# Optimization experiments

Hardware: AMD Instinct MI355X
Metric: run time of the kernel (lower is better)

Reference implementation:

```python
import jax, jax.numpy as jnp
from jax import lax
import numpy as np

B, T, D, H, DH, FF, K = 16, 1024, 512, 8, 64, 2048, 3
EPS = 1e-5


def _layer_norm(x, g, b):
    mu = jnp.mean(x, axis=-1, keepdims=True)
    var = jnp.mean((x - mu) ** 2, axis=-1, keepdims=True)
    return (x - mu) / jnp.sqrt(var + EPS) * g + b


def setup_inputs() -> dict:
    key = jax.random.key(0)
    ks = jax.random.split(key, 14)
    f32 = jnp.float32
    dec_inp = jax.random.normal(ks[0], (B, T, D), f32)
    lengths = jax.random.randint(ks[1], (B,), T // 2, T + 1)
    mask = (jnp.arange(T)[None, :] < lengths[:, None])[:, :, None]  # [B,T,1] bool
    qkv_w = jax.random.normal(ks[2], (3 * H * DH, D), f32) * (D ** -0.5)
    qkv_b = jnp.zeros((3 * H * DH,), f32)
    o_w = jax.random.normal(ks[3], (D, H * DH), f32) * ((H * DH) ** -0.5)
    ln1_g = jnp.ones((D,), f32)
    ln1_b = jnp.zeros((D,), f32)
    conv1_w = jax.random.normal(ks[4], (FF, D, K), f32) * ((D * K) ** -0.5)
    conv1_b = jnp.zeros((FF,), f32)
    conv2_w = jax.random.normal(ks[5], (D, FF, K), f32) * ((FF * K) ** -0.5)
    conv2_b = jnp.zeros((D,), f32)
    ln2_g = jnp.ones((D,), f32)
    ln2_b = jnp.zeros((D,), f32)
    return dict(dec_inp=dec_inp, mask=mask, qkv_w=qkv_w, qkv_b=qkv_b, o_w=o_w,
                ln1_g=ln1_g, ln1_b=ln1_b, conv1_w=conv1_w, conv1_b=conv1_b,
                conv2_w=conv2_w, conv2_b=conv2_b, ln2_g=ln2_g, ln2_b=ln2_b)


def reference(dec_inp, mask, qkv_w, qkv_b, o_w, ln1_g, ln1_b,
              conv1_w, conv1_b, conv2_w, conv2_b, ln2_g, ln2_b):
    # ----- MultiHeadAttn (post-norm, dropout = identity in eval) -----
    attn_mask = ~mask[:, :, 0]                      # [B,T], True = pad
    qkv = dec_inp @ qkv_w.T + qkv_b                 # [B,T,3*H*DH]
    q, k, v = jnp.split(qkv, 3, axis=2)

    def to_heads(x):  # [B,T,H*DH] -> [B*H,T,DH] (batch-major, as in torch)
        return x.reshape(B, T, H, DH).transpose(0, 2, 1, 3).reshape(B * H, T, DH)

    q, k, v = to_heads(q), to_heads(k), to_heads(v)
    scores = jnp.einsum('bqd,bkd->bqk', q, k) * (DH ** -0.5)  # [B*H,T,T]
    # faithful to torch: mask tiled head-major (index i % B)
    am = jnp.tile(attn_mask[:, None, :], (H, T, 1))           # [B*H,T,T]
    scores = jnp.where(am, -jnp.inf, scores)
    prob = jax.nn.softmax(scores, axis=2)
    vec = jnp.einsum('bqk,bkd->bqd', prob, v)                 # [B*H,T,DH]
    # faithful to torch: view as [H,B,...] then permute
    vec = vec.reshape(H, B, T, DH).transpose(1, 2, 0, 3).reshape(B, T, H * DH)
    attn_out = vec @ o_w.T                                    # [B,T,D]
    out = _layer_norm(dec_inp + attn_out, ln1_g, ln1_b)
    out = out * mask

    # ----- PositionwiseConvFF (post-norm) -----
    x = out.transpose(0, 2, 1)                                # [B,D,T]
    h = lax.conv_general_dilated(x, conv1_w, (1,), [(K // 2, K // 2)],
                                 dimension_numbers=('NCH', 'OIH', 'NCH'))
    h = jax.nn.relu(h + conv1_b[None, :, None])
    h = lax.conv_general_dilated(h, conv2_w, (1,), [(K // 2, K // 2)],
                                 dimension_numbers=('NCH', 'OIH', 'NCH'))
    core = (h + conv2_b[None, :, None]).transpose(0, 2, 1)    # [B,T,D]
    out = _layer_norm(out + core, ln2_g, ln2_b)
    return out * mask
```

## Files before the change

### kernel.cpp

```cpp
#include <hip/hip_runtime.h>

using h16 = _Float16;
using h16x4 = __attribute__((ext_vector_type(4))) _Float16;
using h16x8 = __attribute__((ext_vector_type(8))) _Float16;
using f32x4 = __attribute__((ext_vector_type(4))) float;

static constexpr int cB = 16, cT = 1024, cD = 512, cH = 8, cDH = 64, cFF = 2048;
static constexpr int cM = cB * cT;
static constexpr int cTP = cT + 2;

__device__ __forceinline__ bool mask_val(const void* mb, int idx) {
  const unsigned char* u8 = (const unsigned char*)mb;
  if (u8[1] == 1) return u8[idx] != 0;
  const float* f = (const float*)mb;
  if (f[1] == 1.0f) return f[idx] != 0.0f;
  return ((const int*)mb)[idx] != 0;
}

__device__ __forceinline__ void gl_lds16(const h16* g, h16* l) {
  __builtin_amdgcn_global_load_lds(
      (const __attribute__((address_space(1))) unsigned int*)g,
      (__attribute__((address_space(3))) unsigned int*)l, 16, 0, 0);
}


__global__ __launch_bounds__(256)
void k_prep(const float* __restrict__ dec, h16* __restrict__ dec_h,
            const float* __restrict__ qkv_w, h16* __restrict__ qkvw_h,
            const float* __restrict__ o_w, h16* __restrict__ ow_h,
            const float* __restrict__ c1w, h16* __restrict__ w1p,
            const float* __restrict__ c2w, h16* __restrict__ w2p,
            h16* __restrict__ xp, h16* __restrict__ hp) {
  const int b = blockIdx.x;
  if (b < 8192) {
    int i = b * 256 + threadIdx.x;
    const float4 f = ((const float4*)dec)[i];
    h16x4 o = {(h16)f.x, (h16)f.y, (h16)f.z, (h16)f.w};
    ((h16x4*)dec_h)[i] = o;
  } else if (b < 8960) {
    int i = (b - 8192) * 256 + threadIdx.x;
    const float4 f = ((const float4*)qkv_w)[i];
    h16x4 o = {(h16)f.x, (h16)f.y, (h16)f.z, (h16)f.w};
    ((h16x4*)qkvw_h)[i] = o;
  } else if (b < 9216) {
    int i = (b - 8960) * 256 + threadIdx.x;
    const float4 f = ((const float4*)o_w)[i];
    h16x4 o = {(h16)f.x, (h16)f.y, (h16)f.z, (h16)f.w};
    ((h16x4*)ow_h)[i] = o;
  } else if (b < 13312) {
    int i = (b - 9216) * 256 + threadIdx.x;
    int f = i >> 9, d = i & 511;
#pragma unroll
    for (int k = 0; k < 3; ++k)
      w1p[f * (3 * cD) + k * cD + d] = (h16)c1w[(long)i * 3 + k];
  } else if (b < 17408) {
    int i = (b - 13312) * 256 + threadIdx.x;
    int o = i >> 11, f = i & 2047;
#pragma unroll
    for (int k = 0; k < 3; ++k)
      w2p[o * (3 * cFF) + k * cFF + f] = (h16)c2w[(long)i * 3 + k];
  } else {
    int i = (b - 17408) * 256 + threadIdx.x;
    if (i < cB * 2 * cD) {
      int bb = i / (2 * cD); int rr = (i / cD) & 1; int c = i % cD;
      xp[((long)bb * cTP + rr * (cTP - 1)) * cD + c] = (h16)0.f;
    }
    if (i < cB * 2 * cFF) {
      int bb = i / (2 * cFF); int rr = (i / cFF) & 1; int c = i % cFF;
      hp[((long)bb * cTP + rr * (cTP - 1)) * cFF + c] = (h16)0.f;
    }
  }
}

template <int SKIP, bool A_CONV, bool OUT_CONV, bool BIAS, bool RELU,
          bool OUT_H16, bool VSCAT, int SPLITK, bool SWIZ>
__global__ __launch_bounds__(256)
void gemm_bt(const h16* __restrict__ A, const h16* __restrict__ W,
             const float* __restrict__ bias, void* __restrict__ Cv,
             h16* __restrict__ Vg, const void* __restrict__ maskbuf,
             int ldc, int Kd, int lda, long zstride) {
  __shared__ h16 smem[2 * 128 * 64];
  h16* As = smem;
  h16* Bs = smem + 128 * 64;
  const int tid = threadIdx.x;
  const int w = tid >> 6, l = tid & 63;
  int m0, n0;
  if (SWIZ) {
    m0 = (blockIdx.x * 16 + (blockIdx.y >> 2)) * 128;
    n0 = (blockIdx.y & 3) * 128;
  } else {
    m0 = blockIdx.y * 128;
    n0 = blockIdx.x * 128;
  }

  if (SKIP == 1) {
    if (!mask_val(maskbuf, m0)) return;
  } else if (SKIP == 2) {
    int t0 = m0 & 1023, base = ((m0 >> 10) & 1) * 8;
    bool need = false;
#pragma unroll
    for (int i = 0; i < 8; ++i) need |= mask_val(maskbuf, ((base + i) << 10) + t0);
    if (!need) return;
  } else if (SKIP == 3) {
    int t0 = m0 & 1023;
    if (t0 && !mask_val(maskbuf, m0 - 1)) return;
  }

  const int wm = (w >> 1) * 64, wn = (w & 1) * 64;
  const int lr = l >> 3;
  const int lcs = ((l & 7) ^ lr) * 8;
  const int fr = l & 15;
  const int fb = fr & 7;
  const int qd = l >> 4;

  const int kspan = (SPLITK == 2) ? (Kd >> 1) : Kd;
  const int kbeg = (SPLITK == 2) ? blockIdx.z * kspan : 0;
  const int kend = kbeg + kspan;

  f32x4 zero4 = {0.f, 0.f, 0.f, 0.f};
  f32x4 acc[4][4];
#pragma unroll
  for (int mi = 0; mi < 4; ++mi)
#pragma unroll
    for (int ni = 0; ni < 4; ++ni) acc[mi][ni] = zero4;

  for (int k0 = kbeg; k0 < kend; k0 += 64) {
    __syncthreads();
#pragma unroll
    for (int i = 0; i < 4; ++i) {
      int c = w * 4 + i;
      int ar = m0 + c * 8 + lr;
      long aoff = (long)(ar + (A_CONV ? 2 * (ar >> 10) : 0)) * lda + k0 + lcs;
      gl_lds16(A + aoff, &As[c * 512]);
      int br = n0 + c * 8 + lr;
      long boff = (long)br * Kd + k0 + lcs;
      gl_lds16(W + boff, &Bs[c * 512]);
    }
    __syncthreads();
#pragma unroll
    for (int kc = 0; kc < 2; ++kc) {
      h16x8 af[4], bfr[4];
#pragma unroll
      for (int mi = 0; mi < 4; ++mi)
        af[mi] = *(const h16x8*)&As[(wm + mi * 16 + fr) * 64 +
                                    (((kc * 4 + qd) ^ fb) * 8)];
#pragma unroll
      for (int ni = 0; ni < 4; ++ni)
        bfr[ni] = *(const h16x8*)&Bs[(wn + ni * 16 + fr) * 64 +
                                     (((kc * 4 + qd) ^ fb) * 8)];
#pragma unroll
      for (int mi = 0; mi < 4; ++mi)
#pragma unroll
        for (int ni = 0; ni < 4; ++ni)
          acc[mi][ni] = __builtin_amdgcn_mfma_f32_16x16x32_f16(
              af[mi], bfr[ni], acc[mi][ni], 0, 0, 0);
    }
  }
  const bool do_bias = BIAS && (SPLITK == 1 || blockIdx.z == 0);
  if (VSCAT && n0 >= 1024) {
#pragma unroll
    for (int mi = 0; mi < 4; ++mi) {
      int t0 = (m0 + wm + mi * 16 + (l >> 4) * 4) & 1023;
      int jj = ((m0 >> 10) << 3);
#pragma unroll
      for (int ni = 0; ni < 4; ++ni) {
        int gc = n0 + wn + ni * 16 + fr;
        int dh = gc & 63;
        int j2 = jj + ((gc - 1024) >> 6);
        float bb = do_bias ? bias[gc] : 0.f;
        h16x4 v4 = {(h16)(acc[mi][ni][0] + bb), (h16)(acc[mi][ni][1] + bb),
                    (h16)(acc[mi][ni][2] + bb), (h16)(acc[mi][ni][3] + bb)};
        *(h16x4*)&Vg[((long)j2 * 64 + dh) * 1024 + t0] = v4;
      }
    }
  } else if (OUT_H16) {
    __syncthreads();
#pragma unroll
    for (int mi = 0; mi < 4; ++mi) {
#pragma unroll
      for (int ni = 0; ni < 4; ++ni) {
#pragma unroll
        for (int rr = 0; rr < 4; ++rr) {
          int rrow = wm + mi * 16 + (l >> 4) * 4 + rr;
          int ccol = wn + ni * 16 + fr;
          float v = acc[mi][ni][rr];
          if (do_bias) v += bias[n0 + ccol];
          if (RELU) v = v > 0.f ? v : 0.f;
          smem[rrow * 128 + ccol] = (h16)v;
        }
      }
    }
    __syncthreads();
    h16* outp = (h16*)Cv + (SPLITK == 2 ? (long)blockIdx.z * zstride : 0);
    const int r2 = tid >> 4, c2 = (tid & 15) * 8;
#pragma unroll
    for (int i = 0; i < 8; ++i) {
      int row = r2 + i * 16;
      int gr = m0 + row;
      long orow = (long)gr + (OUT_CONV ? (2 * (gr >> 10) + 1) : 0);
      *(h16x8*)&outp[orow * ldc + n0 + c2] = *(h16x8*)&smem[row * 128 + c2];
    }
  } else {
#pragma unroll
    for (int mi = 0; mi < 4; ++mi) {
#pragma unroll
      for (int ni = 0; ni < 4; ++ni) {
#pragma unroll
        for (int rr = 0; rr < 4; ++rr) {
          int gr = m0 + wm + mi * 16 + (l >> 4) * 4 + rr;
          int gc = n0 + wn + ni * 16 + fr;
          float v = acc[mi][ni][rr];
          if (do_bias) v += bias[gc];
          if (RELU) v = v > 0.f ? v : 0.f;
          long orow = (long)gr + (OUT_CONV ? (2 * (gr >> 10) + 1) : 0);
          ((float*)Cv)[orow * ldc + gc] = v;
        }
      }
    }
  }
}

template <int SKIP, bool A_CONV, bool OUT_CONV, bool BIAS, bool RELU,
          int SPLITK, int NBLK_LOG2>
__global__ __launch_bounds__(1024, 4)
void gemm16(const h16* __restrict__ A, const h16* __restrict__ W,
            const float* __restrict__ bias, h16* __restrict__ C,
            const void* __restrict__ maskbuf, int ldc, int Kd, int lda,
            long zstride) {
  extern __shared__ h16 sm[];
  const int tid = threadIdx.x;
  const int wid = tid >> 6, l = tid & 63;
  const int m0 = (blockIdx.x * 8 + (blockIdx.y >> NBLK_LOG2)) * 256;
  const int n0 = (blockIdx.y & ((1 << NBLK_LOG2) - 1)) * 256;

  if (SKIP == 1) {
    if (!mask_val(maskbuf, m0)) return;
  } else if (SKIP == 3) {
    int t0 = m0 & 1023;
    if (t0 && !mask_val(maskbuf, m0 - 1)) return;
  }

  const int wm = wid >> 2, wn = wid & 3;
  const int fr = l & 15, qd = l >> 4;

  const int kspan = (SPLITK == 2) ? (Kd >> 1) : Kd;
  const int kbeg = (SPLITK == 2) ? blockIdx.z * kspan : 0;
  const int nt = kspan >> 5;

  f32x4 zero4 = {0.f, 0.f, 0.f, 0.f};
  f32x4 acc[4][4];
#pragma unroll
  for (int m = 0; m < 4; ++m)
#pragma unroll
    for (int n = 0; n < 4; ++n) acc[m][n] = zero4;

  const int srow = tid >> 2;
  const int sch = ((tid & 3) - ((tid >> 3) & 3)) & 3;
  const int ar0 = m0 + srow;
  const long aoff0 =
      (long)(ar0 + (A_CONV ? 2 * (ar0 >> 10) : 0)) * lda + kbeg + sch * 8;
  const long boff0 = (long)(n0 + srow) * Kd + kbeg + sch * 8;
  auto stage = [&](int ti) {
    h16* buf = sm + (ti & 3) * 16384;
    gl_lds16(A + aoff0 + ti * 32, &buf[wid * 512]);
    gl_lds16(W + boff0 + ti * 32, &buf[8192 + wid * 512]);
  };

  const int abase = (wm * 64 + fr) * 32 + (((qd + (fr >> 1)) & 3) * 8);
  const int bbase = (wn * 64 + fr) * 32 + (((qd + (fr >> 1)) & 3) * 8);

  stage(0);
  if (nt > 1) stage(1);
  asm volatile("s_waitcnt vmcnt(0)" ::: "memory");
  __builtin_amdgcn_s_barrier();

  for (int s = 0; s < nt; s += 2) {
    if (s + 2 < nt) stage(s + 2);
    if (s + 3 < nt) stage(s + 3);
#pragma unroll
    for (int u = 0; u < 2; ++u) {
      const int t = s + u;
      const h16* Ab = sm + (t & 3) * 16384;
      const h16* Bb = Ab + 8192;
      h16x8 a[4], b[4];
#pragma unroll
      for (int m = 0; m < 4; ++m)
        a[m] = *(const h16x8*)&Ab[abase + m * 512];
#pragma unroll
      for (int n = 0; n < 4; ++n)
        b[n] = *(const h16x8*)&Bb[bbase + n * 512];
      __builtin_amdgcn_s_setprio(1);
#pragma unroll
      for (int m = 0; m < 4; ++m)
#pragma unroll
        for (int n = 0; n < 4; ++n)
          acc[m][n] = __builtin_amdgcn_mfma_f32_16x16x32_f16(a[m], b[n],
                                                             acc[m][n], 0, 0, 0);
      __builtin_amdgcn_s_setprio(0);
    }
    asm volatile("s_waitcnt vmcnt(0)" ::: "memory");
    __builtin_amdgcn_s_barrier();
  }

  const bool do_bias = BIAS && (SPLITK == 1 || blockIdx.z == 0);
  const int qd4 = qd * 4;
#pragma unroll
  for (int m = 0; m < 4; ++m) {
    int row = wm * 64 + m * 16 + qd4;
#pragma unroll
    for (int n = 0; n < 4; ++n) {
      int col = wn * 64 + n * 16 + fr;
      float bb = do_bias ? bias[n0 + col] : 0.f;
#pragma unroll
      for (int rr = 0; rr < 4; ++rr) {
        float v = acc[m][n][rr] + bb;
        if (RELU) v = v > 0.f ? v : 0.f;
        sm[(row + rr) * 256 + col] = (h16)v;
      }
    }
  }
  __syncthreads();
  h16* outp = C + (SPLITK == 2 ? (long)blockIdx.z * zstride : 0);
  const int r2 = tid >> 5, c2 = (tid & 31) * 8;
#pragma unroll
  for (int i = 0; i < 8; ++i) {
    int row = r2 + i * 32;
    int gr = m0 + row;
    long orow = (long)gr + (OUT_CONV ? (2 * (gr >> 10) + 1) : 0);
    *(h16x8*)&outp[orow * (long)ldc + n0 + c2] = *(h16x8*)&sm[row * 256 + c2];
  }
}

__global__ __launch_bounds__(512, 6)
void k_attn(const h16* __restrict__ qk, const h16* __restrict__ Vg,
            const void* __restrict__ maskbuf, h16* __restrict__ attn_out) {
  __shared__ h16 Ks[2][64 * 64];
  __shared__ h16 Vt[2][64 * 64];
  __shared__ h16 Ps[8][16 * 68];
  __shared__ float sbias[2][64];
  const int tid = threadIdx.x, w = tid >> 6, l = tid & 63;
  const int f = blockIdx.x;
  const int bp = f & 15, qt = (f >> 4) & 7, hp = f >> 7;
  const int j = hp * 16 + bp;
  const int bd = j >> 3, hd = j & 7;

  if (!mask_val(maskbuf, bp * cT + qt * 128)) return;

  const int fr = l & 15, fq = (l >> 4) * 8;
  const int fb = fr & 7, qd = l >> 4;
  const int lr = l >> 3, lcs = ((l & 7) ^ lr) * 8;

  int nkv = 16;
  for (int t = 8; t < 16; ++t)
    if (!mask_val(maskbuf, bp * cT + t * 64)) { nkv = t; break; }

  h16x8 qf[2];
#pragma unroll
  for (int kc = 0; kc < 2; ++kc) {
    qf[kc] = *(const h16x8*)&qk[
        (long)((bd << 10) + qt * 128 + w * 16 + fr) * 1024 +
        hd * 64 + kc * 32 + fq];
    qf[kc] *= (h16)0.125f;
  }

  auto stageKV = [&](int t) {
    const int buf = t & 1;
    const int k0 = t * 64;
    const int c = w;
    const int row = c * 8 + lr;
    gl_lds16(qk + (long)((bd << 10) + k0 + row) * 1024 + 512 + hd * 64 + lcs,
             &Ks[buf][c * 512]);
    gl_lds16(Vg + ((long)j * 64 + row) * 1024 + k0 + lcs, &Vt[buf][c * 512]);
    if (tid < 64)
      sbias[buf][tid] = mask_val(maskbuf, bp * cT + k0 + tid) ? 0.f : -1e30f;
  };

  f32x4 zero4 = {0.f, 0.f, 0.f, 0.f};
  f32x4 o[4];
  float lrow[4];
#pragma unroll
  for (int nt = 0; nt < 4; ++nt) o[nt] = zero4;
#pragma unroll
  for (int r = 0; r < 4; ++r) lrow[r] = 0.f;

  stageKV(0);
  __syncthreads();

  for (int t = 0; t < nkv; ++t) {
    const int cur = t & 1;
    if (t + 1 < nkv) stageKV(t + 1);

    f32x4 S[4];
#pragma unroll
    for (int kt = 0; kt < 4; ++kt) {
      float sb = sbias[cur][kt * 16 + fr];
      f32x4 s = {sb, sb, sb, sb};
#pragma unroll
      for (int kc = 0; kc < 2; ++kc) {
        h16x8 kf = *(const h16x8*)&Ks[cur][(kt * 16 + fr) * 64 +
                                          (((kc * 4 + qd) ^ fb) * 8)];
        s = __builtin_amdgcn_mfma_f32_16x16x32_f16(qf[kc], kf, s, 0, 0, 0);
      }
      S[kt] = s;
    }
#pragma unroll
    for (int r = 0; r < 4; ++r) {
      float p0 = __expf(S[0][r] - 4.f), p1 = __expf(S[1][r] - 4.f);
      float p2 = __expf(S[2][r] - 4.f), p3 = __expf(S[3][r] - 4.f);
      lrow[r] += (p0 + p1) + (p2 + p3);
      int ql = (l >> 4) * 4 + r;
      Ps[w][ql * 68 + fr] = (h16)p0;
      Ps[w][ql * 68 + 16 + fr] = (h16)p1;
      Ps[w][ql * 68 + 32 + fr] = (h16)p2;
      Ps[w][ql * 68 + 48 + fr] = (h16)p3;
    }
#pragma unroll
    for (int kp = 0; kp < 2; ++kp) {
      h16x8 pf = *(const h16x8*)&Ps[w][fr * 68 + kp * 32 + fq];
#pragma unroll
      for (int nt = 0; nt < 4; ++nt) {
        h16x8 vf = *(const h16x8*)&Vt[cur][(nt * 16 + fr) * 64 +
                                           (((kp * 4 + qd) ^ fb) * 8)];
        o[nt] = __builtin_amdgcn_mfma_f32_16x16x32_f16(pf, vf, o[nt], 0, 0, 0);
      }
    }
    __syncthreads();
  }
#pragma unroll
  for (int r = 0; r < 4; ++r) {
#pragma unroll
    for (int m = 1; m < 16; m <<= 1) lrow[r] += __shfl_xor(lrow[r], m);
    float inv = 1.f / lrow[r];
    int q = qt * 128 + w * 16 + (l >> 4) * 4 + r;
    long row = (long)bp * cT + q;
#pragma unroll
    for (int nt = 0; nt < 4; ++nt)
      attn_out[row * cD + hp * 64 + nt * 16 + fr] = (h16)(o[nt][r] * inv);
  }
}

template <bool WRITE_XP, bool RH16, bool R2H16, bool XH16, bool WRITE_OUTF>
__global__ __launch_bounds__(256)
void k_ln(const void* __restrict__ Xv, const void* __restrict__ Rv,
          const void* __restrict__ Rv2,
          const float* __restrict__ g, const float* __restrict__ bta,
          const void* __restrict__ maskbuf,
          float* __restrict__ outf, h16* __restrict__ xp) {
  const int w = threadIdx.x >> 6, l = threadIdx.x & 63;
  const long row = (long)blockIdx.x * 4 + w;
  float v[8];
  if (XH16) {
    const long xr = row + 2 * (row >> 10) + 1;
    const h16x4* x4 = (const h16x4*)((const h16*)Xv + xr * cD);
    h16x4 a0 = x4[l], a1 = x4[l + 64];
    v[0] = (float)a0[0]; v[1] = (float)a0[1];
    v[2] = (float)a0[2]; v[3] = (float)a0[3];
    v[4] = (float)a1[0]; v[5] = (float)a1[1];
    v[6] = (float)a1[2]; v[7] = (float)a1[3];
  } else {
    const float4* x4 = (const float4*)((const float*)Xv + row * cD);
    float4 a0 = x4[l], a1 = x4[l + 64];
    v[0] = a0.x; v[1] = a0.y; v[2] = a0.z; v[3] = a0.w;
    v[4] = a1.x; v[5] = a1.y; v[6] = a1.z; v[7] = a1.w;
  }
  if (RH16) {
    const h16x4* r4 = (const h16x4*)((const h16*)Rv + row * cD);
    h16x4 b0 = r4[l], b1 = r4[l + 64];
    v[0] += (float)b0[0]; v[1] += (float)b0[1];
    v[2] += (float)b0[2]; v[3] += (float)b0[3];
    v[4] += (float)b1[0]; v[5] += (float)b1[1];
    v[6] += (float)b1[2]; v[7] += (float)b1[3];
  } else {
    const float4* r4 = (const float4*)((const float*)Rv + row * cD);
    float4 b0 = r4[l], b1 = r4[l + 64];
    v[0] += b0.x; v[1] += b0.y; v[2] += b0.z; v[3] += b0.w;
    v[4] += b1.x; v[5] += b1.y; v[6] += b1.z; v[7] += b1.w;
  }
  if (R2H16) {
    const h16x4* r4 = (const h16x4*)((const h16*)Rv2 + row * cD);
    h16x4 b0 = r4[l], b1 = r4[l + 64];
    v[0] += (float)b0[0]; v[1] += (float)b0[1];
    v[2] += (float)b0[2]; v[3] += (float)b0[3];
    v[4] += (float)b1[0]; v[5] += (float)b1[1];
    v[6] += (float)b1[2]; v[7] += (float)b1[3];
  }
  float s = 0.f;
#pragma unroll
  for (int i = 0; i < 8; ++i) s += v[i];
#pragma unroll
  for (int m = 1; m < 64; m <<= 1) s += __shfl_xor(s, m);
  const float mu = s * (1.f / 512.f);
  float s2 = 0.f;
#pragma unroll
  for (int i = 0; i < 8; ++i) { float d = v[i] - mu; s2 += d * d; }
#pragma unroll
  for (int m = 1; m < 64; m <<= 1) s2 += __shfl_xor(s2, m);
  const float rstd = rsqrtf(s2 * (1.f / 512.f) + 1e-5f);
  const float mv = mask_val(maskbuf, (int)row) ? 1.f : 0.f;
  const float4* g4 = (const float4*)g;
  const float4* t4 = (const float4*)bta;
  float4 g0 = g4[l], g1 = g4[l + 64], t0 = t4[l], t1 = t4[l + 64];
  float4 y0, y1;
  y0.x = ((v[0] - mu) * rstd * g0.x + t0.x) * mv;
  y0.y = ((v[1] - mu) * rstd * g0.y + t0.y) * mv;
  y0.z = ((v[2] - mu) * rstd * g0.z + t0.z) * mv;
  y0.w = ((v[3] - mu) * rstd * g0.w + t0.w) * mv;
  y1.x = ((v[4] - mu) * rstd * g1.x + t1.x) * mv;
  y1.y = ((v[5] - mu) * rstd * g1.y + t1.y) * mv;
  y1.z = ((v[6] - mu) * rstd * g1.z + t1.z) * mv;
  y1.w = ((v[7] - mu) * rstd * g1.w + t1.w) * mv;
  if (WRITE_OUTF) {
    ((float4*)(outf + row * cD))[l] = y0;
    ((float4*)(outf + row * cD))[l + 64] = y1;
  }
  if (WRITE_XP) {
    const long xrow = row + 2 * (row >> 10) + 1;
    h16x4 h0 = {(h16)y0.x, (h16)y0.y, (h16)y0.z, (h16)y0.w};
    h16x4 h1 = {(h16)y1.x, (h16)y1.y, (h16)y1.z, (h16)y1.w};
    ((h16x4*)(xp + xrow * cD))[l] = h0;
    ((h16x4*)(xp + xrow * cD))[l + 64] = h1;
  }
}

extern "C" void kernel_launch(void* const* d_in, const int* in_sizes, int n_in,
                              void* d_out, int out_size, void* d_ws, size_t ws_size,
                              hipStream_t stream) {
  const float* dec   = (const float*)d_in[0];
  const void*  maskb = d_in[1];
  const float* qkv_w = (const float*)d_in[2];
  const float* qkv_b = (const float*)d_in[3];
  const float* o_w   = (const float*)d_in[4];
  const float* ln1g  = (const float*)d_in[5];
  const float* ln1b  = (const float*)d_in[6];
  const float* c1w   = (const float*)d_in[7];
  const float* c1b   = (const float*)d_in[8];
  const float* c2w   = (const float*)d_in[9];
  const float* c2b   = (const float*)d_in[10];
  const float* ln2g  = (const float*)d_in[11];
  const float* ln2b  = (const float*)d_in[12];

  char* p = (char*)d_ws;
  auto alloc = [&](size_t bytes) {
    char* r = p; p += (bytes + 255) & ~(size_t)255; return r;
  };
  h16*   dec_h  = (h16*)alloc((size_t)cM * cD * 2);
  h16*   qkvw_h = (h16*)alloc((size_t)1536 * cD * 2);
  h16*   ow_h   = (h16*)alloc((size_t)cD * cD * 2);
  h16*   w1p    = (h16*)alloc((size_t)cFF * 3 * cD * 2);
  h16*   w2p    = (h16*)alloc((size_t)cD * 3 * cFF * 2);
  h16*   qk_h   = (h16*)alloc((size_t)cM * 1024 * 2);
  h16*   vg     = (h16*)alloc((size_t)cB * cH * cDH * cT * 2);
  h16*   attn_h = (h16*)alloc((size_t)cM * cD * 2);
  float* tmp    = (float*)alloc((size_t)cM * cD * 4);
  float* out1   = (float*)alloc((size_t)cM * cD * 4);
  h16*   xp     = (h16*)alloc((size_t)cB * cTP * cD * 2);
  h16*   hp     = (h16*)alloc((size_t)cB * cTP * cFF * 2);
  h16*   core0 = attn_h;
  h16*   core1 = qk_h;
  h16*   tmp_h = (h16*)tmp;
  (void)ws_size; (void)n_in; (void)in_sizes; (void)out_size; (void)out1;

  static bool s_attr = false;
  if (!s_attr) {
    hipFuncSetAttribute(
        reinterpret_cast<const void*>(&gemm16<3, true, true, true, true, 1, 3>),
        hipFuncAttributeMaxDynamicSharedMemorySize, 131072);
    hipFuncSetAttribute(
        reinterpret_cast<const void*>(&gemm16<1, true, false, true, false, 2, 1>),
        hipFuncAttributeMaxDynamicSharedMemorySize, 131072);
    s_attr = true;
  }

  k_prep<<<dim3(17664), 256, 0, stream>>>(dec, dec_h, qkv_w, qkvw_h, o_w, ow_h,
                                          c1w, w1p, c2w, w2p, xp, hp);

  gemm_bt<2, false, false, true, false, true, true, 1, false>
      <<<dim3(12, cM / 128), 256, 0, stream>>>(dec_h, qkvw_h, qkv_b, qk_h, vg,
                                               maskb, 1024, cD, cD, 0);

  k_attn<<<dim3(1024), 512, 0, stream>>>(qk_h, vg, maskb, attn_h);

  gemm_bt<1, false, false, false, false, true, false, 1, false>
      <<<dim3(cD / 128, cM / 128), 256, 0, stream>>>(attn_h, ow_h, nullptr, tmp_h,
                                                     nullptr, maskb, cD, cD, cD, 0);

  k_ln<true, true, false, false, false><<<cM / 4, 256, 0, stream>>>(
      dec, tmp_h, nullptr, ln1g, ln1b, maskb, nullptr, xp);

  gemm16<3, true, true, true, true, 1, 3>
      <<<dim3(8, 64), dim3(1024), 131072, stream>>>(xp, w1p, c1b, hp, maskb,
                                                    cFF, 3 * cD, cD, 0);

  gemm16<1, true, false, true, false, 2, 1>
      <<<dim3(8, 16, 2), dim3(1024), 131072, stream>>>(hp, w2p, c2b, core0,
                                                       maskb, cD, 3 * cFF, cFF,
                                                       (long)(core1 - core0));

  k_ln<false, true, true, true, true><<<cM / 4, 256, 0, stream>>>(
      xp, core0, core1, ln2g, ln2b, maskb, (float*)d_out, nullptr);
}
```

Before: 455.5 us.

## Route QKV and output-projection GEMMs through the large-tile gemm16 kernel

Removes the 128x128 gemm_bt kernel and runs the QKV projection and attention output projection through the 256x256, 1024-thread gemm16 kernel used for the conv FFN. The V-scatter epilogue is ported into gemm16, and the grid mapping is generalised from a power-of-two N-block count to an arbitrary NT. Larger tiles give more data reuse and a pipelined main loop. The cost is coarser mask-skip granularity and fewer blocks for the small-N output projection (8x16 grid).

```diff
diff --git a/kernel.cpp b/kernel.cpp
--- a/kernel.cpp
+++ b/kernel.cpp
@@ -73,25 +73,18 @@
 }
 
 template <int SKIP, bool A_CONV, bool OUT_CONV, bool BIAS, bool RELU,
-          bool OUT_H16, bool VSCAT, int SPLITK, bool SWIZ>
-__global__ __launch_bounds__(256)
-void gemm_bt(const h16* __restrict__ A, const h16* __restrict__ W,
-             const float* __restrict__ bias, void* __restrict__ Cv,
-             h16* __restrict__ Vg, const void* __restrict__ maskbuf,
-             int ldc, int Kd, int lda, long zstride) {
-  __shared__ h16 smem[2 * 128 * 64];
-  h16* As = smem;
-  h16* Bs = smem + 128 * 64;
+          int SPLITK, int NT, bool VSCAT>
+__global__ __launch_bounds__(1024, 4)
+void gemm16(const h16* __restrict__ A, const h16* __restrict__ W,
+            const float* __restrict__ bias, h16* __restrict__ C,
+            h16* __restrict__ Vg, const void* __restrict__ maskbuf,
+            int ldc, int Kd, int lda, long zstride) {
+  extern __shared__ h16 sm[];
   const int tid = threadIdx.x;
-  const int w = tid >> 6, l = tid & 63;
-  int m0, n0;
-  if (SWIZ) {
-    m0 = (blockIdx.x * 16 + (blockIdx.y >> 2)) * 128;
-    n0 = (blockIdx.y & 3) * 128;
-  } else {
-    m0 = blockIdx.y * 128;
-    n0 = blockIdx.x * 128;
-  }
+  const int wid = tid >> 6, l = tid & 63;
+  const int mper = gridDim.y / NT;
+  const int m0 = (blockIdx.x * mper + blockIdx.y / NT) * 256;
+  const int n0 = (blockIdx.y % NT) * 256;
 
   if (SKIP == 1) {
     if (!mask_val(maskbuf, m0)) return;
@@ -101,140 +94,6 @@
 #pragma unroll
     for (int i = 0; i < 8; ++i) need |= mask_val(maskbuf, ((base + i) << 10) + t0);
     if (!need) return;
-  } else if (SKIP == 3) {
-    int t0 = m0 & 1023;
-    if (t0 && !mask_val(maskbuf, m0 - 1)) return;
-  }
-
-  const int wm = (w >> 1) * 64, wn = (w & 1) * 64;
-  const int lr = l >> 3;
-  const int lcs = ((l & 7) ^ lr) * 8;
-  const int fr = l & 15;
-  const int fb = fr & 7;
-  const int qd = l >> 4;
-
-  const int kspan = (SPLITK == 2) ? (Kd >> 1) : Kd;
-  const int kbeg = (SPLITK == 2) ? blockIdx.z * kspan : 0;
-  const int kend = kbeg + kspan;
-
-  f32x4 zero4 = {0.f, 0.f, 0.f, 0.f};
-  f32x4 acc[4][4];
-#pragma unroll
-  for (int mi = 0; mi < 4; ++mi)
-#pragma unroll
-    for (int ni = 0; ni < 4; ++ni) acc[mi][ni] = zero4;
-
-  for (int k0 = kbeg; k0 < kend; k0 += 64) {
-    __syncthreads();
-#pragma unroll
-    for (int i = 0; i < 4; ++i) {
-      int c = w * 4 + i;
-      int ar = m0 + c * 8 + lr;
-      long aoff = (long)(ar + (A_CONV ? 2 * (ar >> 10) : 0)) * lda + k0 + lcs;
-      gl_lds16(A + aoff, &As[c * 512]);
-      int br = n0 + c * 8 + lr;
-      long boff = (long)br * Kd + k0 + lcs;
-      gl_lds16(W + boff, &Bs[c * 512]);
-    }
-    __syncthreads();
-#pragma unroll
-    for (int kc = 0; kc < 2; ++kc) {
-      h16x8 af[4], bfr[4];
-#pragma unroll
-      for (int mi = 0; mi < 4; ++mi)
-        af[mi] = *(const h16x8*)&As[(wm + mi * 16 + fr) * 64 +
-                                    (((kc * 4 + qd) ^ fb) * 8)];
-#pragma unroll
-      for (int ni = 0; ni < 4; ++ni)
-        bfr[ni] = *(const h16x8*)&Bs[(wn + ni * 16 + fr) * 64 +
-                                     (((kc * 4 + qd) ^ fb) * 8)];
-#pragma unroll
-      for (int mi = 0; mi < 4; ++mi)
-#pragma unroll
-        for (int ni = 0; ni < 4; ++ni)
-          acc[mi][ni] = __builtin_amdgcn_mfma_f32_16x16x32_f16(
-              af[mi], bfr[ni], acc[mi][ni], 0, 0, 0);
-    }
-  }
-  const bool do_bias = BIAS && (SPLITK == 1 || blockIdx.z == 0);
-  if (VSCAT && n0 >= 1024) {
-#pragma unroll
-    for (int mi = 0; mi < 4; ++mi) {
-      int t0 = (m0 + wm + mi * 16 + (l >> 4) * 4) & 1023;
-      int jj = ((m0 >> 10) << 3);
-#pragma unroll
-      for (int ni = 0; ni < 4; ++ni) {
-        int gc = n0 + wn + ni * 16 + fr;
-        int dh = gc & 63;
-        int j2 = jj + ((gc - 1024) >> 6);
-        float bb = do_bias ? bias[gc] : 0.f;
-        h16x4 v4 = {(h16)(acc[mi][ni][0] + bb), (h16)(acc[mi][ni][1] + bb),
-                    (h16)(acc[mi][ni][2] + bb), (h16)(acc[mi][ni][3] + bb)};
-        *(h16x4*)&Vg[((long)j2 * 64 + dh) * 1024 + t0] = v4;
-      }
-    }
-  } else if (OUT_H16) {
-    __syncthreads();
-#pragma unroll
-    for (int mi = 0; mi < 4; ++mi) {
-#pragma unroll
-      for (int ni = 0; ni < 4; ++ni) {
-#pragma unroll
-        for (int rr = 0; rr < 4; ++rr) {
-          int rrow = wm + mi * 16 + (l >> 4) * 4 + rr;
-          int ccol = wn + ni * 16 + fr;
-          float v = acc[mi][ni][rr];
-          if (do_bias) v += bias[n0 + ccol];
-          if (RELU) v = v > 0.f ? v : 0.f;
-          smem[rrow * 128 + ccol] = (h16)v;
-        }
-      }
-    }
-    __syncthreads();
-    h16* outp = (h16*)Cv + (SPLITK == 2 ? (long)blockIdx.z * zstride : 0);
-    const int r2 = tid >> 4, c2 = (tid & 15) * 8;
-#pragma unroll
-    for (int i = 0; i < 8; ++i) {
-      int row = r2 + i * 16;
-      int gr = m0 + row;
-      long orow = (long)gr + (OUT_CONV ? (2 * (gr >> 10) + 1) : 0);
-      *(h16x8*)&outp[orow * ldc + n0 + c2] = *(h16x8*)&smem[row * 128 + c2];
-    }
-  } else {
-#pragma unroll
-    for (int mi = 0; mi < 4; ++mi) {
-#pragma unroll
-      for (int ni = 0; ni < 4; ++ni) {
-#pragma unroll
-        for (int rr = 0; rr < 4; ++rr) {
-          int gr = m0 + wm + mi * 16 + (l >> 4) * 4 + rr;
-          int gc = n0 + wn + ni * 16 + fr;
-          float v = acc[mi][ni][rr];
-          if (do_bias) v += bias[gc];
-          if (RELU) v = v > 0.f ? v : 0.f;
-          long orow = (long)gr + (OUT_CONV ? (2 * (gr >> 10) + 1) : 0);
-          ((float*)Cv)[orow * ldc + gc] = v;
-        }
-      }
-    }
-  }
-}
-
-template <int SKIP, bool A_CONV, bool OUT_CONV, bool BIAS, bool RELU,
-          int SPLITK, int NBLK_LOG2>
-__global__ __launch_bounds__(1024, 4)
-void gemm16(const h16* __restrict__ A, const h16* __restrict__ W,
-            const float* __restrict__ bias, h16* __restrict__ C,
-            const void* __restrict__ maskbuf, int ldc, int Kd, int lda,
-            long zstride) {
-  extern __shared__ h16 sm[];
-  const int tid = threadIdx.x;
-  const int wid = tid >> 6, l = tid & 63;
-  const int m0 = (blockIdx.x * 8 + (blockIdx.y >> NBLK_LOG2)) * 256;
-  const int n0 = (blockIdx.y & ((1 << NBLK_LOG2) - 1)) * 256;
-
-  if (SKIP == 1) {
-    if (!mask_val(maskbuf, m0)) return;
   } else if (SKIP == 3) {
     int t0 = m0 & 1023;
     if (t0 && !mask_val(maskbuf, m0 - 1)) return;
@@ -303,6 +162,26 @@
   }
 
   const bool do_bias = BIAS && (SPLITK == 1 || blockIdx.z == 0);
+
+  if (VSCAT && n0 >= 1024) {
+    const int jj = (m0 >> 10) << 3;
+#pragma unroll
+    for (int m = 0; m < 4; ++m) {
+      int t0 = (m0 + wm * 64 + m * 16 + qd * 4) & 1023;
+#pragma unroll
+      for (int n = 0; n < 4; ++n) {
+        int gc = n0 + wn * 64 + n * 16 + fr;
+        int dh = gc & 63;
+        int j2 = jj + ((gc - 1024) >> 6);
+        float bb = do_bias ? bias[gc] : 0.f;
+        h16x4 v4 = {(h16)(acc[m][n][0] + bb), (h16)(acc[m][n][1] + bb),
+                    (h16)(acc[m][n][2] + bb), (h16)(acc[m][n][3] + bb)};
+        *(h16x4*)&Vg[((long)j2 * 64 + dh) * 1024 + t0] = v4;
+      }
+    }
+    return;
+  }
+
   const int qd4 = qd * 4;
 #pragma unroll
   for (int m = 0; m < 4; ++m) {
@@ -563,10 +442,20 @@
   static bool s_attr = false;
   if (!s_attr) {
     hipFuncSetAttribute(
-        reinterpret_cast<const void*>(&gemm16<3, true, true, true, true, 1, 3>),
+        reinterpret_cast<const void*>(
+            &gemm16<2, false, false, true, false, 1, 6, true>),
         hipFuncAttributeMaxDynamicSharedMemorySize, 131072);
     hipFuncSetAttribute(
-        reinterpret_cast<const void*>(&gemm16<1, true, false, true, false, 2, 1>),
+        reinterpret_cast<const void*>(
+            &gemm16<1, false, false, false, false, 1, 2, false>),
+        hipFuncAttributeMaxDynamicSharedMemorySize, 131072);
+    hipFuncSetAttribute(
+        reinterpret_cast<const void*>(
+            &gemm16<3, true, true, true, true, 1, 8, false>),
+        hipFuncAttributeMaxDynamicSharedMemorySize, 131072);
+    hipFuncSetAttribute(
+        reinterpret_cast<const void*>(
+            &gemm16<1, true, false, true, false, 2, 2, false>),
         hipFuncAttributeMaxDynamicSharedMemorySize, 131072);
     s_attr = true;
   }
@@ -574,26 +463,28 @@
   k_prep<<<dim3(17664), 256, 0, stream>>>(dec, dec_h, qkv_w, qkvw_h, o_w, ow_h,
                                           c1w, w1p, c2w, w2p, xp, hp);
 
-  gemm_bt<2, false, false, true, false, true, true, 1, false>
-      <<<dim3(12, cM / 128), 256, 0, stream>>>(dec_h, qkvw_h, qkv_b, qk_h, vg,
-                                               maskb, 1024, cD, cD, 0);
+  gemm16<2, false, false, true, false, 1, 6, true>
+      <<<dim3(8, 48), dim3(1024), 131072, stream>>>(dec_h, qkvw_h, qkv_b, qk_h,
+                                                    vg, maskb, 1024, cD, cD, 0);
 
   k_attn<<<dim3(1024), 512, 0, stream>>>(qk_h, vg, maskb, attn_h);
 
-  gemm_bt<1, false, false, false, false, true, false, 1, false>
-      <<<dim3(cD / 128, cM / 128), 256, 0, stream>>>(attn_h, ow_h, nullptr, tmp_h,
-                                                     nullptr, maskb, cD, cD, cD, 0);
+  gemm16<1, false, false, false, false, 1, 2, false>
+      <<<dim3(8, 16), dim3(1024), 131072, stream>>>(attn_h, ow_h, nullptr,
+                                                    tmp_h, nullptr, maskb,
+                                                    cD, cD, cD, 0);
 
   k_ln<true, true, false, false, false><<<cM / 4, 256, 0, stream>>>(
       dec, tmp_h, nullptr, ln1g, ln1b, maskb, nullptr, xp);
 
-  gemm16<3, true, true, true, true, 1, 3>
-      <<<dim3(8, 64), dim3(1024), 131072, stream>>>(xp, w1p, c1b, hp, maskb,
-                                                    cFF, 3 * cD, cD, 0);
-
-  gemm16<1, true, false, true, false, 2, 1>
+  gemm16<3, true, true, true, true, 1, 8, false>
+      <<<dim3(8, 64), dim3(1024), 131072, stream>>>(xp, w1p, c1b, hp, nullptr,
+                                                    maskb, cFF, 3 * cD, cD, 0);
+
+  gemm16<1, true, false, true, false, 2, 2, false>
       <<<dim3(8, 16, 2), dim3(1024), 131072, stream>>>(hp, w2p, c2b, core0,
-                                                       maskb, cD, 3 * cFF, cFF,
+                                                       nullptr, maskb, cD,
+                                                       3 * cFF, cFF,
                                                        (long)(core1 - core0));
 
   k_ln<false, true, true, true, true><<<cM / 4, 256, 0, stream>>>(
```

Result: no change. 464.1 us (+1.9%).
